# Kernel tuning notes

Hardware: AMD Instinct MI355X
Metric: run time of the kernel (lower is better)

Reference implementation:

```python
import jax, jax.numpy as jnp
import numpy as np
from jax import lax

B, Hs, Ws = 2, 256, 256
DIM = 256        # query channels (c)
DIM_BAK = 256    # key/value channels (c2)
HEADS = 8
WIN = 8
HEAD_DIM = DIM // HEADS
SCALE = HEAD_DIM ** -0.5


def window_partition(x, ws):
    # x: [B, H, W, C] -> [B*nH*nW, ws, ws, C]
    b, h, w, c = x.shape
    x = x.reshape(b, h // ws, ws, w // ws, ws, c)
    return x.transpose(0, 1, 3, 2, 4, 5).reshape(-1, ws, ws, c)


def window_reverse(windows, ws, h, w):
    # windows: [B*nH*nW, ws, ws, C] -> [B, H, W, C]
    b = windows.shape[0] // ((h // ws) * (w // ws))
    x = windows.reshape(b, h // ws, w // ws, ws, ws, -1)
    return x.transpose(0, 1, 3, 2, 4, 5).reshape(b, h, w, -1)


def setup_inputs() -> dict:
    key = jax.random.key(0)
    ks = jax.random.split(key, 9)
    s = 0.02
    return {
        "query_feature": jax.random.normal(ks[0], (B, DIM, Hs, Ws), jnp.float32),
        "key_value_feature": jax.random.normal(ks[1], (B, DIM_BAK, Hs, Ws), jnp.float32),
        # depthwise 3x3 conv on kv (groups=DIM_BAK, bias=False): OIHW with I=1
        "w_dw": jax.random.normal(ks[2], (DIM_BAK, 1, 3, 3), jnp.float32) * s,
        # to_q: Linear(dim -> dim), stored [in, out]
        "wq": jax.random.normal(ks[3], (DIM, DIM), jnp.float32) * s,
        "bq": jax.random.normal(ks[4], (DIM,), jnp.float32) * s,
        # to_kv: Linear(dim_bak -> 2*dim)
        "wkv": jax.random.normal(ks[5], (DIM_BAK, 2 * DIM), jnp.float32) * s,
        "bkv": jax.random.normal(ks[6], (2 * DIM,), jnp.float32) * s,
        # project_out: Linear(dim -> dim)
        "w_proj": jax.random.normal(ks[7], (DIM, DIM), jnp.float32) * s,
        "b_proj": jax.random.normal(ks[8], (DIM,), jnp.float32) * s,
    }


def reference(query_feature, key_value_feature, w_dw, wq, bq, wkv, bkv, w_proj, b_proj):
    b, c, h, w = query_feature.shape
    c2 = key_value_feature.shape[1]

    # depthwise 3x3 conv on key/value feature (padding=1, stride=1)
    kv = lax.conv_general_dilated(
        key_value_feature, w_dw,
        window_strides=(1, 1), padding="SAME",
        feature_group_count=c2,
        dimension_numbers=("NCHW", "OIHW", "NCHW"))

    # NCHW -> NHWC, partition into non-overlapping windows
    qw = window_partition(query_feature.transpose(0, 2, 3, 1), WIN)  # [B_, ws, ws, c]
    kvw = window_partition(kv.transpose(0, 2, 3, 1), WIN)            # [B_, ws, ws, c2]
    B_ = qw.shape[0]
    N = WIN * WIN
    qw = qw.reshape(B_, N, c)
    kvw = kvw.reshape(B_, N, c2)

    # projections -> multi-head [B_, heads, N, head_dim]
    q = (qw @ wq + bq).reshape(B_, N, HEADS, HEAD_DIM).transpose(0, 2, 1, 3) * SCALE
    kv_proj = (kvw @ wkv + bkv).reshape(B_, N, 2, HEADS, HEAD_DIM)
    k = kv_proj[:, :, 0].transpose(0, 2, 1, 3)
    v = kv_proj[:, :, 1].transpose(0, 2, 1, 3)

    # windowed cross-attention
    attn = jax.nn.softmax(jnp.einsum("bhnd,bhmd->bhnm", q, k), axis=-1)
    out = jnp.einsum("bhnm,bhmd->bhnd", attn, v)
    out = out.transpose(0, 2, 1, 3).reshape(B_, N, c)
    out = out @ w_proj + b_proj

    # reverse windows, back to NCHW
    out = window_reverse(out.reshape(B_, WIN, WIN, c), WIN, h, w)
    return out.transpose(0, 3, 1, 2)
```

## Files before the change

kernel.cpp:

```cpp
#include <hip/hip_runtime.h>
#include <hip/hip_bf16.h>
#include <cstdint>
#include <cstddef>

typedef __hip_bfloat16 bf16;
typedef short bf16x8 __attribute__((ext_vector_type(8)));
typedef float f32x4 __attribute__((ext_vector_type(4)));

#define MFMA(a, b, c) __builtin_amdgcn_mfma_f32_16x16x32_bf16((a), (b), (c), 0, 0, 0)

__global__ __launch_bounds__(256) void wtrans_k(const float* __restrict__ wq,
                                                const float* __restrict__ wkv,
                                                const float* __restrict__ wp,
                                                bf16* __restrict__ wqT,
                                                bf16* __restrict__ wkvT,
                                                bf16* __restrict__ wpT) {
  int idx = blockIdx.x * 256 + threadIdx.x;
  if (idx < 65536) {
    int n = idx >> 8, k = idx & 255;
    wqT[idx] = __float2bfloat16(wq[k * 256 + n]);
  } else if (idx < 196608) {
    int i = idx - 65536;
    int n = i >> 8, k = i & 255;
    wkvT[i] = __float2bfloat16(wkv[k * 512 + n]);
  } else {
    int i = idx - 196608;
    int n = i >> 8, k = i & 255;
    wpT[i] = __float2bfloat16(wp[k * 256 + n]);
  }
}

__global__ __launch_bounds__(256) void t_winq_k(const float* __restrict__ src,
                                                bf16* __restrict__ dst,
                                                int hw0, int swoff) {
  __shared__ bf16 T[64][66];
  int tile = blockIdx.x;
  int c0 = (tile & 3) << 6;
  int hwb = hw0 + ((tile >> 2) << 6);
  int tid = threadIdx.x;
  {
    int hwl = tid & 63, cb = tid >> 6;
    const float* s = src + (size_t)(c0 + cb) * 65536 + hwb + hwl;
#pragma unroll
    for (int i = 0; i < 16; ++i)
      T[cb + i * 4][hwl] = __float2bfloat16(s[(size_t)i * 4 * 65536]);
  }
  __syncthreads();
  {
    int cl = tid & 63, hb = tid >> 6;
#pragma unroll
    for (int j = 0; j < 16; ++j) {
      int hwl = hb + j * 4;
      int hw = hwb + hwl;
      int h = hw >> 8, w = hw & 255;
      int sw = swoff + ((h >> 3) << 5) + (w >> 3);
      int t = ((h & 7) << 3) + (w & 7);
      dst[((size_t)(sw * 64 + t) << 8) + c0 + cl] = T[cl][hwl];
    }
  }
}

__global__ __launch_bounds__(256) void t_nhwc_k(const float* __restrict__ src,
                                                bf16* __restrict__ dst) {
  __shared__ bf16 T[64][66];
  int tile = blockIdx.x;
  int c0 = (tile & 3) << 6;
  int hwoff = (tile >> 2) << 6;
  int tid = threadIdx.x;
  {
    int hwl = tid & 63, cb = tid >> 6;
    const float* s = src + (size_t)(c0 + cb) * 65536 + hwoff + hwl;
#pragma unroll
    for (int i = 0; i < 16; ++i)
      T[cb + i * 4][hwl] = __float2bfloat16(s[(size_t)i * 4 * 65536]);
  }
  __syncthreads();
  {
    int cl = tid & 63, hb = tid >> 6;
#pragma unroll
    for (int j = 0; j < 16; ++j) {
      int hwl = hb + j * 4;
      dst[((size_t)(hwoff + hwl) << 8) + c0 + cl] = T[cl][hwl];
    }
  }
}

__global__ __launch_bounds__(256) void convkv_k(const bf16* __restrict__ SK,
                                                const float* __restrict__ wdw,
                                                const bf16* __restrict__ wkvT,
                                                const float* __restrict__ bkv,
                                                bf16* __restrict__ k_s,
                                                bf16* __restrict__ vT_s,
                                                int wid_base, int cnt, int psw0,
                                                int nwtot) {
  __shared__ __align__(16) bf16 X[64 * 264];
  int bid = blockIdx.x;
  int swc = (bid & 7) * (cnt >> 3) + (bid >> 3);
  int sw = psw0 + swc;
  int wid = wid_base + swc;
  int rem = wid & 1023, wh = rem >> 5, ww = rem & 31;
  int h0 = wh * 8, w0 = ww * 8;
  int tid = threadIdx.x;
  {
    int c = tid;
    float wr[9];
#pragma unroll
    for (int q = 0; q < 9; ++q) wr[q] = wdw[c * 9 + q];
    const bool wlo = (w0 > 0), whi = (w0 < 248);
    float rows[3][10];
    auto load_row = [&](int gh, float* r) {
      if (gh >= 0 && gh < 256) {
        const bf16* rp = SK + ((size_t)(gh * 256 + w0) << 8) + c;
        r[0] = wlo ? __bfloat162float(rp[-256]) : 0.f;
#pragma unroll
        for (int s = 1; s <= 8; ++s) r[s] = __bfloat162float(rp[(s - 1) * 256]);
        r[9] = whi ? __bfloat162float(rp[8 * 256]) : 0.f;
      } else {
#pragma unroll
        for (int e = 0; e < 10; ++e) r[e] = 0.f;
      }
    };
    load_row(h0 - 1, rows[0]);
    load_row(h0, rows[1]);
#pragma unroll
    for (int i = 0; i < 8; ++i) {
      load_row(h0 + i + 1, rows[(i + 2) % 3]);
#pragma unroll
      for (int j = 0; j < 8; ++j) {
        float acc = 0.f;
#pragma unroll
        for (int di = 0; di < 3; ++di) {
          const float* rp = rows[(i + di) % 3];
          acc = __builtin_fmaf(wr[di * 3 + 0], rp[j], acc);
          acc = __builtin_fmaf(wr[di * 3 + 1], rp[j + 1], acc);
          acc = __builtin_fmaf(wr[di * 3 + 2], rp[j + 2], acc);
        }
        X[(i * 8 + j) * 264 + c] = __float2bfloat16(acc);
      }
    }
  }
  __syncthreads();
  int wave = tid >> 6, lane = tid & 63, quad = lane >> 4, l16 = lane & 15;
  int n0 = wave * 64;
  f32x4 zero4 = {0.f, 0.f, 0.f, 0.f};
  f32x4 acc[4][4];
  for (int mt = 0; mt < 4; ++mt)
    for (int nt = 0; nt < 4; ++nt) acc[mt][nt] = zero4;
  for (int k0 = 0; k0 < 256; k0 += 32) {
    bf16x8 a[4], bb[4];
    for (int mt = 0; mt < 4; ++mt)
      a[mt] = *(const bf16x8*)&X[(mt * 16 + l16) * 264 + k0 + quad * 8];
    for (int nt = 0; nt < 4; ++nt)
      bb[nt] = *(const bf16x8*)&wkvT[(size_t)(n0 + nt * 16 + l16) * 256 + k0 + quad * 8];
    for (int mt = 0; mt < 4; ++mt)
      for (int nt = 0; nt < 4; ++nt) acc[mt][nt] = MFMA(a[mt], bb[nt], acc[mt][nt]);
  }
  for (int nt = 0; nt < 4; ++nt) {
    int n = n0 + nt * 16 + l16;
    float bias = bkv[n];
    for (int mt = 0; mt < 4; ++mt) {
      int mb = mt * 16 + quad * 4;
      for (int r = 0; r < 4; ++r)
        k_s[((size_t)(sw * 64 + mb + r) << 8) + n] =
            __float2bfloat16(acc[mt][nt][r] + bias);
    }
  }
  for (int mt = 0; mt < 4; ++mt)
    for (int nt = 0; nt < 4; ++nt) acc[mt][nt] = zero4;
  for (int k0 = 0; k0 < 256; k0 += 32) {
    bf16x8 a[4], bb[4];
    for (int mt = 0; mt < 4; ++mt)
      a[mt] = *(const bf16x8*)&X[(mt * 16 + l16) * 264 + k0 + quad * 8];
    for (int nt = 0; nt < 4; ++nt)
      bb[nt] = *(const bf16x8*)&wkvT[(size_t)(256 + n0 + nt * 16 + l16) * 256 + k0 + quad * 8];
    for (int mt = 0; mt < 4; ++mt)
      for (int nt = 0; nt < 4; ++nt) acc[mt][nt] = MFMA(bb[nt], a[mt], acc[mt][nt]);
  }
  for (int nt = 0; nt < 4; ++nt) {
    for (int r = 0; r < 4; ++r) {
      int vd = n0 + nt * 16 + quad * 4 + r;
      float bias = bkv[256 + vd];
      for (int mt = 0; mt < 4; ++mt)
        vT_s[((size_t)(sw * 256 + vd) << 6) + mt * 16 + l16] =
            __float2bfloat16(acc[mt][nt][r] + bias);
    }
  }
}

__global__ __launch_bounds__(256) void fused_k(const bf16* __restrict__ qwM,
                                               const bf16* __restrict__ wqT,
                                               const float* __restrict__ bq,
                                               const bf16* __restrict__ k_s,
                                               const bf16* __restrict__ vT_s,
                                               const bf16* __restrict__ wpT,
                                               const float* __restrict__ bp,
                                               float* __restrict__ out,
                                               int wid_base, int nw) {
  __shared__ __align__(16) bf16 Q[64 * 264];
  __shared__ __align__(16) bf16 P[4 * 64 * 72];
  int bid = blockIdx.x;
  int sw = (bid & 7) * (nw >> 3) + (bid >> 3);
  int wid = wid_base + sw;
  int b = wid >> 10, rem = wid & 1023, wh = rem >> 5, ww = rem & 31;
  int h0 = wh * 8, w0 = ww * 8;
  int tid = threadIdx.x, wave = tid >> 6, lane = tid & 63, quad = lane >> 4, l16 = lane & 15;
  f32x4 zero4 = {0.f, 0.f, 0.f, 0.f};
  {
    int t = tid >> 2, cb = (tid & 3) * 64;
    const bf16* src = &qwM[((size_t)(sw * 64 + t) << 8) + cb];
    bf16* dst = &P[t * 264 + cb];
    for (int i = 0; i < 8; ++i) *(bf16x8*)&dst[i * 8] = *(const bf16x8*)&src[i * 8];
  }
  __syncthreads();
  {
    const bf16* Xq = P;
    int n0 = wave * 64;
    f32x4 acc[4][4];
    for (int mt = 0; mt < 4; ++mt)
      for (int nt = 0; nt < 4; ++nt) acc[mt][nt] = zero4;
    for (int k0 = 0; k0 < 256; k0 += 32) {
      bf16x8 a[4], bb[4];
      for (int mt = 0; mt < 4; ++mt)
        a[mt] = *(const bf16x8*)&Xq[(mt * 16 + l16) * 264 + k0 + quad * 8];
      for (int nt = 0; nt < 4; ++nt)
        bb[nt] = *(const bf16x8*)&wqT[(size_t)(n0 + nt * 16 + l16) * 256 + k0 + quad * 8];
      for (int mt = 0; mt < 4; ++mt)
        for (int nt = 0; nt < 4; ++nt) acc[mt][nt] = MFMA(a[mt], bb[nt], acc[mt][nt]);
    }
    const float scale = 0.1767766952966369f;
    for (int nt = 0; nt < 4; ++nt) {
      int n = n0 + nt * 16 + l16;
      float bias = bq[n];
      for (int mt = 0; mt < 4; ++mt) {
        int mb = mt * 16 + quad * 4;
        for (int r = 0; r < 4; ++r)
          Q[(mb + r) * 264 + n] = __float2bfloat16((acc[mt][nt][r] + bias) * scale);
      }
    }
  }
  __syncthreads();
  const bf16* kw = k_s + ((size_t)sw << 14);
  const bf16* vw = vT_s + ((size_t)sw << 14);
  bf16* Pw = P + wave * 64 * 72;
  for (int hi = 0; hi < 2; ++hi) {
    int co = (wave + hi * 4) * 32;
    f32x4 s[4][4];
    for (int mt = 0; mt < 4; ++mt)
      for (int nt = 0; nt < 4; ++nt) s[mt][nt] = zero4;
    {
      bf16x8 a[4], bb[4];
      for (int mt = 0; mt < 4; ++mt)
        a[mt] = *(const bf16x8*)&Q[(mt * 16 + l16) * 264 + co + quad * 8];
      for (int nt = 0; nt < 4; ++nt)
        bb[nt] = *(const bf16x8*)&kw[(size_t)(nt * 16 + l16) * 256 + co + quad * 8];
      for (int mt = 0; mt < 4; ++mt)
        for (int nt = 0; nt < 4; ++nt) s[mt][nt] = MFMA(a[mt], bb[nt], s[mt][nt]);
    }
    float rsum[4][4];
    for (int mt = 0; mt < 4; ++mt) {
      for (int r = 0; r < 4; ++r) {
        float m = s[mt][0][r];
        for (int nt = 1; nt < 4; ++nt) m = fmaxf(m, s[mt][nt][r]);
        m = fmaxf(m, __shfl_xor(m, 1, 64));
        m = fmaxf(m, __shfl_xor(m, 2, 64));
        m = fmaxf(m, __shfl_xor(m, 4, 64));
        m = fmaxf(m, __shfl_xor(m, 8, 64));
        float sum = 0.f;
        for (int nt = 0; nt < 4; ++nt) {
          float e = __expf(s[mt][nt][r] - m);
          s[mt][nt][r] = e;
          sum += e;
        }
        sum += __shfl_xor(sum, 1, 64);
        sum += __shfl_xor(sum, 2, 64);
        sum += __shfl_xor(sum, 4, 64);
        sum += __shfl_xor(sum, 8, 64);
        rsum[mt][r] = sum;
      }
    }
    for (int mt = 0; mt < 4; ++mt)
      for (int nt = 0; nt < 4; ++nt)
        for (int r = 0; r < 4; ++r)
          Pw[(mt * 16 + quad * 4 + r) * 72 + nt * 16 + l16] =
              __float2bfloat16(s[mt][nt][r]);
    __syncthreads();
    f32x4 o[4][2];
    for (int mt = 0; mt < 4; ++mt)
      for (int nt = 0; nt < 2; ++nt) o[mt][nt] = zero4;
    for (int kk = 0; kk < 64; kk += 32) {
      bf16x8 pa[4], vb[2];
      for (int mt = 0; mt < 4; ++mt)
        pa[mt] = *(const bf16x8*)&Pw[(mt * 16 + l16) * 72 + kk + quad * 8];
      for (int nt = 0; nt < 2; ++nt)
        vb[nt] = *(const bf16x8*)&vw[(size_t)(co + nt * 16 + l16) * 64 + kk + quad * 8];
      for (int mt = 0; mt < 4; ++mt)
        for (int nt = 0; nt < 2; ++nt) o[mt][nt] = MFMA(pa[mt], vb[nt], o[mt][nt]);
    }
    for (int mt = 0; mt < 4; ++mt) {
      int mb = mt * 16 + quad * 4;
      for (int nt = 0; nt < 2; ++nt)
        for (int r = 0; r < 4; ++r)
          Q[(mb + r) * 264 + co + nt * 16 + l16] =
              __float2bfloat16(o[mt][nt][r] / rsum[mt][r]);
    }
    __syncthreads();
  }
  {
    int n0 = wave * 64;
    f32x4 acc[4][4];
    for (int mt = 0; mt < 4; ++mt)
      for (int nt = 0; nt < 4; ++nt) acc[mt][nt] = zero4;
    for (int k0 = 0; k0 < 256; k0 += 32) {
      bf16x8 a[4], bb[4];
      for (int mt = 0; mt < 4; ++mt)
        a[mt] = *(const bf16x8*)&Q[(mt * 16 + l16) * 264 + k0 + quad * 8];
      for (int nt = 0; nt < 4; ++nt)
        bb[nt] = *(const bf16x8*)&wpT[(size_t)(n0 + nt * 16 + l16) * 256 + k0 + quad * 8];
      for (int mt = 0; mt < 4; ++mt)
        for (int nt = 0; nt < 4; ++nt) acc[mt][nt] = MFMA(a[mt], bb[nt], acc[mt][nt]);
    }
    for (int nt = 0; nt < 4; ++nt) {
      int n = n0 + nt * 16 + l16;
      float bias = bp[n];
      float* chan = out + ((size_t)(b * 256 + n) << 16);
      for (int mt = 0; mt < 4; ++mt) {
        int row_i = mt * 2 + (quad >> 1);
        int j0 = (quad & 1) * 4;
        f32x4 v4;
        for (int r = 0; r < 4; ++r) v4[r] = acc[mt][nt][r] + bias;
        *(f32x4*)&chan[(size_t)(h0 + row_i) * 256 + w0 + j0] = v4;
      }
    }
  }
}

extern "C" void kernel_launch(void* const* d_in, const int* in_sizes, int n_in,
                              void* d_out, int out_size, void* d_ws, size_t ws_size,
                              hipStream_t stream) {
  const float* qf  = (const float*)d_in[0];
  const float* kvf = (const float*)d_in[1];
  const float* wdw = (const float*)d_in[2];
  const float* wq  = (const float*)d_in[3];
  const float* bq  = (const float*)d_in[4];
  const float* wkv = (const float*)d_in[5];
  const float* bkv = (const float*)d_in[6];
  const float* wp  = (const float*)d_in[7];
  const float* bp  = (const float*)d_in[8];
  float* out = (float*)d_out;

  bf16* wqT  = (bf16*)d_ws;
  bf16* wkvT = wqT + 65536;
  bf16* wpT  = wkvT + 131072;
  bf16* bufs = wpT + 65536;
  const size_t welems = 65536 + 131072 + 65536;
  const size_t skelems = (size_t)256 * 256 * 256;

  int passes = 1;
  while (passes < 32) {
    size_t nw_ = 2048 / passes;
    size_t elems = welems + skelems + 3 * nw_ * 16384;
    if (elems * 2 <= ws_size) break;
    passes <<= 1;
  }
  int nw = 2048 / passes;
  size_t sz = (size_t)nw * 16384;
  bf16* SK  = bufs;
  bf16* qwM = SK + skelems;
  bf16* KS  = qwM + sz;
  bf16* VT  = KS + sz;

  wtrans_k<<<1024, 256, 0, stream>>>(wq, wkv, wp, wqT, wkvT, wpT);

  for (int p = 0; p < passes; ++p) {
    int wbP = p * nw;
    int b0 = wbP >> 10, b1 = (wbP + nw - 1) >> 10;
    for (int b = b0; b <= b1; ++b) {
      int s = wbP > b * 1024 ? wbP : b * 1024;
      int e = (wbP + nw) < (b + 1) * 1024 ? (wbP + nw) : (b + 1) * 1024;
      int cnt = e - s;
      int h0 = ((s & 1023) >> 5) * 8;
      t_winq_k<<<cnt * 4, 256, 0, stream>>>(qf + ((size_t)b << 24), qwM,
                                            h0 * 256, b * 1024 - wbP);
    }
    for (int b = b0; b <= b1; ++b) {
      int s = wbP > b * 1024 ? wbP : b * 1024;
      int e = (wbP + nw) < (b + 1) * 1024 ? (wbP + nw) : (b + 1) * 1024;
      int cnt = e - s;
      t_nhwc_k<<<4096, 256, 0, stream>>>(kvf + ((size_t)b << 24), SK);
      convkv_k<<<cnt, 256, 0, stream>>>(SK, wdw, wkvT, bkv, KS, VT,
                                        s, cnt, s - wbP, nw);
    }
    fused_k<<<nw, 256, 0, stream>>>(qwM, wqT, bq, KS, VT, wpT, bp, out, wbP, nw);
  }
}
```

Before: 620.7 us.

## Make attention stages wave-private with XOR-swizzled LDS to drop block barriers

The Q projection now reads activations straight from global memory instead of staging them in LDS. Each wave computes Q only for the two heads it later attends over and keeps the result in a wave-private, XOR-swizzled LDS tile. This removes all but one __syncthreads between the projection, the softmax and PV stages, and also cuts LDS from about 70 KB to 48 KB so that three blocks can fit per CU (launch_bounds 256,3). The P buffer is split into half-width chunks. The conv/kv kernel's X tile swaps its padded layout for an XOR swizzle. The risks are more global reads for the Q input, register pressure from the occupancy hint, and wave-level LDS hazards that are now left without barriers.

```diff
diff --git a/kernel.cpp b/kernel.cpp
--- a/kernel.cpp
+++ b/kernel.cpp
@@ -93,7 +93,12 @@
                                                 bf16* __restrict__ vT_s,
                                                 int wid_base, int cnt, int psw0,
                                                 int nwtot) {
-  __shared__ __align__(16) bf16 X[64 * 264];
+  __shared__ __align__(16) bf16 X[64 * 256];
+  auto xp = [&](int row, int col) -> bf16* {
+    int by = (row << 9) + (col << 1);
+    by ^= (row & 7) << 4;
+    return (bf16*)((char*)X + by);
+  };
   int bid = blockIdx.x;
   int swc = (bid & 7) * (cnt >> 3) + (bid >> 3);
   int sw = psw0 + swc;
@@ -135,7 +140,7 @@
           acc = __builtin_fmaf(wr[di * 3 + 1], rp[j + 1], acc);
           acc = __builtin_fmaf(wr[di * 3 + 2], rp[j + 2], acc);
         }
-        X[(i * 8 + j) * 264 + c] = __float2bfloat16(acc);
+        *xp(i * 8 + j, c) = __float2bfloat16(acc);
       }
     }
   }
@@ -149,7 +154,7 @@
   for (int k0 = 0; k0 < 256; k0 += 32) {
     bf16x8 a[4], bb[4];
     for (int mt = 0; mt < 4; ++mt)
-      a[mt] = *(const bf16x8*)&X[(mt * 16 + l16) * 264 + k0 + quad * 8];
+      a[mt] = *(const bf16x8*)xp(mt * 16 + l16, k0 + quad * 8);
     for (int nt = 0; nt < 4; ++nt)
       bb[nt] = *(const bf16x8*)&wkvT[(size_t)(n0 + nt * 16 + l16) * 256 + k0 + quad * 8];
     for (int mt = 0; mt < 4; ++mt)
@@ -170,7 +175,7 @@
   for (int k0 = 0; k0 < 256; k0 += 32) {
     bf16x8 a[4], bb[4];
     for (int mt = 0; mt < 4; ++mt)
-      a[mt] = *(const bf16x8*)&X[(mt * 16 + l16) * 264 + k0 + quad * 8];
+      a[mt] = *(const bf16x8*)xp(mt * 16 + l16, k0 + quad * 8);
     for (int nt = 0; nt < 4; ++nt)
       bb[nt] = *(const bf16x8*)&wkvT[(size_t)(256 + n0 + nt * 16 + l16) * 256 + k0 + quad * 8];
     for (int mt = 0; mt < 4; ++mt)
@@ -187,70 +192,81 @@
   }
 }
 
-__global__ __launch_bounds__(256) void fused_k(const bf16* __restrict__ qwM,
-                                               const bf16* __restrict__ wqT,
-                                               const float* __restrict__ bq,
-                                               const bf16* __restrict__ k_s,
-                                               const bf16* __restrict__ vT_s,
-                                               const bf16* __restrict__ wpT,
-                                               const float* __restrict__ bp,
-                                               float* __restrict__ out,
-                                               int wid_base, int nw) {
-  __shared__ __align__(16) bf16 Q[64 * 264];
-  __shared__ __align__(16) bf16 P[4 * 64 * 72];
+__global__ __launch_bounds__(256, 3) void fused_k(const bf16* __restrict__ qwM,
+                                                  const bf16* __restrict__ wqT,
+                                                  const float* __restrict__ bq,
+                                                  const bf16* __restrict__ k_s,
+                                                  const bf16* __restrict__ vT_s,
+                                                  const bf16* __restrict__ wpT,
+                                                  const float* __restrict__ bp,
+                                                  float* __restrict__ out,
+                                                  int wid_base, int nw) {
+  __shared__ __align__(16) bf16 LA[4 * 64 * 64];
+  __shared__ __align__(16) bf16 LB[4 * 64 * 32];
   int bid = blockIdx.x;
   int sw = (bid & 7) * (nw >> 3) + (bid >> 3);
   int wid = wid_base + sw;
   int b = wid >> 10, rem = wid & 1023, wh = rem >> 5, ww = rem & 31;
   int h0 = wh * 8, w0 = ww * 8;
   int tid = threadIdx.x, wave = tid >> 6, lane = tid & 63, quad = lane >> 4, l16 = lane & 15;
+  char* Abase = (char*)LA + wave * 8192;
+  char* Bbase = (char*)LB + wave * 4096;
+  auto apR = [&](int w, int row, int col) -> bf16* {
+    int by = (row << 7) + (col << 1);
+    by ^= (row & 7) << 4;
+    return (bf16*)((char*)LA + w * 8192 + by);
+  };
+  auto ap = [&](int row, int col) -> bf16* {
+    int by = (row << 7) + (col << 1);
+    by ^= (row & 7) << 4;
+    return (bf16*)(Abase + by);
+  };
+  auto Bp = [&](int row, int col) -> bf16* {
+    int by = (row << 6) + (col << 1);
+    by ^= (row & 3) << 4;
+    return (bf16*)(Bbase + by);
+  };
   f32x4 zero4 = {0.f, 0.f, 0.f, 0.f};
   {
-    int t = tid >> 2, cb = (tid & 3) * 64;
-    const bf16* src = &qwM[((size_t)(sw * 64 + t) << 8) + cb];
-    bf16* dst = &P[t * 264 + cb];
-    for (int i = 0; i < 8; ++i) *(bf16x8*)&dst[i * 8] = *(const bf16x8*)&src[i * 8];
-  }
-  __syncthreads();
-  {
-    const bf16* Xq = P;
-    int n0 = wave * 64;
+    const bf16* Aq = qwM + ((size_t)sw << 14);
     f32x4 acc[4][4];
     for (int mt = 0; mt < 4; ++mt)
       for (int nt = 0; nt < 4; ++nt) acc[mt][nt] = zero4;
     for (int k0 = 0; k0 < 256; k0 += 32) {
       bf16x8 a[4], bb[4];
       for (int mt = 0; mt < 4; ++mt)
-        a[mt] = *(const bf16x8*)&Xq[(mt * 16 + l16) * 264 + k0 + quad * 8];
-      for (int nt = 0; nt < 4; ++nt)
-        bb[nt] = *(const bf16x8*)&wqT[(size_t)(n0 + nt * 16 + l16) * 256 + k0 + quad * 8];
+        a[mt] = *(const bf16x8*)&Aq[(size_t)(mt * 16 + l16) * 256 + k0 + quad * 8];
+      for (int nt = 0; nt < 4; ++nt) {
+        int n = (wave + ((nt >> 1) << 2)) * 32 + (nt & 1) * 16 + l16;
+        bb[nt] = *(const bf16x8*)&wqT[(size_t)n * 256 + k0 + quad * 8];
+      }
       for (int mt = 0; mt < 4; ++mt)
         for (int nt = 0; nt < 4; ++nt) acc[mt][nt] = MFMA(a[mt], bb[nt], acc[mt][nt]);
     }
     const float scale = 0.1767766952966369f;
     for (int nt = 0; nt < 4; ++nt) {
-      int n = n0 + nt * 16 + l16;
+      int n = (wave + ((nt >> 1) << 2)) * 32 + (nt & 1) * 16 + l16;
       float bias = bq[n];
       for (int mt = 0; mt < 4; ++mt) {
         int mb = mt * 16 + quad * 4;
         for (int r = 0; r < 4; ++r)
-          Q[(mb + r) * 264 + n] = __float2bfloat16((acc[mt][nt][r] + bias) * scale);
-      }
-    }
-  }
-  __syncthreads();
+          *ap(mb + r, nt * 16 + l16) =
+              __float2bfloat16((acc[mt][nt][r] + bias) * scale);
+      }
+    }
+  }
   const bf16* kw = k_s + ((size_t)sw << 14);
   const bf16* vw = vT_s + ((size_t)sw << 14);
-  bf16* Pw = P + wave * 64 * 72;
   for (int hi = 0; hi < 2; ++hi) {
     int co = (wave + hi * 4) * 32;
+    int lc = hi * 32;
     f32x4 s[4][4];
     for (int mt = 0; mt < 4; ++mt)
       for (int nt = 0; nt < 4; ++nt) s[mt][nt] = zero4;
     {
       bf16x8 a[4], bb[4];
       for (int mt = 0; mt < 4; ++mt)
-        a[mt] = *(const bf16x8*)&Q[(mt * 16 + l16) * 264 + co + quad * 8];
+        a[mt] = *(const bf16x8*)ap(mt * 16 + l16, lc + quad * 8);
       for (int nt = 0; nt < 4; ++nt)
         bb[nt] = *(const bf16x8*)&kw[(size_t)(nt * 16 + l16) * 256 + co + quad * 8];
       for (int mt = 0; mt < 4; ++mt)
@@ -278,21 +294,20 @@
         rsum[mt][r] = sum;
       }
     }
-    for (int mt = 0; mt < 4; ++mt)
-      for (int nt = 0; nt < 4; ++nt)
-        for (int r = 0; r < 4; ++r)
-          Pw[(mt * 16 + quad * 4 + r) * 72 + nt * 16 + l16] =
-              __float2bfloat16(s[mt][nt][r]);
-    __syncthreads();
     f32x4 o[4][2];
     for (int mt = 0; mt < 4; ++mt)
       for (int nt = 0; nt < 2; ++nt) o[mt][nt] = zero4;
-    for (int kk = 0; kk < 64; kk += 32) {
+    for (int half = 0; half < 2; ++half) {
+      for (int mt = 0; mt < 4; ++mt)
+        for (int nt2 = 0; nt2 < 2; ++nt2)
+          for (int r = 0; r < 4; ++r)
+            *Bp(mt * 16 + quad * 4 + r, nt2 * 16 + l16) =
+                __float2bfloat16(s[mt][half * 2 + nt2][r]);
       bf16x8 pa[4], vb[2];
       for (int mt = 0; mt < 4; ++mt)
-        pa[mt] = *(const bf16x8*)&Pw[(mt * 16 + l16) * 72 + kk + quad * 8];
+        pa[mt] = *(const bf16x8*)Bp(mt * 16 + l16, quad * 8);
       for (int nt = 0; nt < 2; ++nt)
-        vb[nt] = *(const bf16x8*)&vw[(size_t)(co + nt * 16 + l16) * 64 + kk + quad * 8];
+        vb[nt] = *(const bf16x8*)&vw[(size_t)(co + nt * 16 + l16) * 64 + half * 32 + quad * 8];
       for (int mt = 0; mt < 4; ++mt)
         for (int nt = 0; nt < 2; ++nt) o[mt][nt] = MFMA(pa[mt], vb[nt], o[mt][nt]);
     }
@@ -300,20 +315,23 @@
       int mb = mt * 16 + quad * 4;
       for (int nt = 0; nt < 2; ++nt)
         for (int r = 0; r < 4; ++r)
-          Q[(mb + r) * 264 + co + nt * 16 + l16] =
+          *ap(mb + r, lc + nt * 16 + l16) =
               __float2bfloat16(o[mt][nt][r] / rsum[mt][r]);
     }
-    __syncthreads();
-  }
+  }
+  __syncthreads();
   {
     int n0 = wave * 64;
     f32x4 acc[4][4];
     for (int mt = 0; mt < 4; ++mt)
       for (int nt = 0; nt < 4; ++nt) acc[mt][nt] = zero4;
     for (int k0 = 0; k0 < 256; k0 += 32) {
+      int head = k0 >> 5;
+      int rw = head & 3;
+      int lc = (head >> 2) * 32;
       bf16x8 a[4], bb[4];
       for (int mt = 0; mt < 4; ++mt)
-        a[mt] = *(const bf16x8*)&Q[(mt * 16 + l16) * 264 + k0 + quad * 8];
+        a[mt] = *(const bf16x8*)apR(rw, mt * 16 + l16, lc + quad * 8);
       for (int nt = 0; nt < 4; ++nt)
         bb[nt] = *(const bf16x8*)&wpT[(size_t)(n0 + nt * 16 + l16) * 256 + k0 + quad * 8];
       for (int mt = 0; mt < 4; ++mt)
```

Result: no change. 623.5 us (+0.4%).
